# Kernel tuning notes

Hardware: AMD Instinct MI355X
Metric: run time of the kernel (lower is better)

## Reference

```python
import jax, jax.numpy as jnp
import numpy as np

# Mamba2Simple defaults for Mamba2Simple(768, headdim=64)
D_MODEL = 768
D_STATE = 128
D_CONV = 4
EXPAND = 2
HEADDIM = 64
D_INNER = EXPAND * D_MODEL           # 1536
NHEADS = D_INNER // HEADDIM          # 24
CONV_DIM = D_INNER + 2 * D_STATE     # 1792 (x, B, C share the depthwise conv)
D_IN_PROJ = 2 * D_INNER + 2 * D_STATE + NHEADS  # 3352 (z, xBC, dt)
N_LAYERS = 4
IM8 = 64      # 8x8 image tokens
IM64 = 4096   # 64x64 image tokens
L = 1 + IM8 + IM64  # 4161 = s0 + im8 + zoom(im8)
B = 4
EPS = 1e-5


def setup_inputs() -> dict:
    key = jax.random.key(0)
    ks = iter(jax.random.split(key, 40))
    nrm = lambda shape, s=0.02: jax.random.normal(next(ks), shape, jnp.float32) * s
    inp = {
        'im8': jax.random.normal(next(ks), (B, IM8, 3), jnp.float32),
        'im64': jax.random.normal(next(ks), (B, IM64, 3), jnp.float32),
        # RGBToModel / ModelToRGB linear projections
        'from_rgb_w': nrm((3, D_MODEL)),
        'from_rgb_b': jnp.zeros((D_MODEL,), jnp.float32),
        'to_rgb_w': nrm((D_MODEL, 3)),
        'to_rgb_b': jnp.zeros((3,), jnp.float32),
        # learned prefix token and zoom positional suffix
        's0': nrm((1, 1, D_MODEL), 1.0),
        'suffix': nrm((IM64, D_MODEL), 1.0),
        'norm0_w': jnp.ones((D_MODEL,), jnp.float32),
        'norm0_b': jnp.zeros((D_MODEL,), jnp.float32),
        # per-layer (stacked over N_LAYERS) Mamba2 params
        'ln_w': jnp.ones((N_LAYERS, D_MODEL), jnp.float32),
        'ln_b': jnp.zeros((N_LAYERS, D_MODEL), jnp.float32),
        'in_proj_w': nrm((N_LAYERS, D_MODEL, D_IN_PROJ)),
        'conv_w': nrm((N_LAYERS, CONV_DIM, D_CONV), 0.1),
        'conv_b': jnp.zeros((N_LAYERS, CONV_DIM), jnp.float32),
        'dt_bias': nrm((N_LAYERS, NHEADS), 0.1),
        'A_log': jnp.log(jax.random.uniform(next(ks), (N_LAYERS, NHEADS), jnp.float32, 1.0, 16.0)),
        'D': nrm((N_LAYERS, NHEADS), 1.0),
        'gn_w': jnp.ones((N_LAYERS, D_INNER), jnp.float32),
        'out_proj_w': nrm((N_LAYERS, D_INNER, D_MODEL)),
    }
    return inp


def _layernorm(x, w, b):
    mu = jnp.mean(x, axis=-1, keepdims=True)
    var = jnp.mean((x - mu) ** 2, axis=-1, keepdims=True)
    return (x - mu) * jax.lax.rsqrt(var + EPS) * w + b


def _rmsnorm(x, w):
    return x * jax.lax.rsqrt(jnp.mean(x * x, axis=-1, keepdims=True) + EPS) * w


def _causal_conv1d(x, w, b):
    # x: (B, L, C) depthwise causal conv, kernel (C, K)
    xt = x.transpose(0, 2, 1)  # (B, C, L)
    y = jax.lax.conv_general_dilated(
        xt, w[:, None, :], window_strides=(1,), padding=[(D_CONV - 1, 0)],
        dimension_numbers=('NCH', 'OIH', 'NCH'), feature_group_count=w.shape[0])
    return y.transpose(0, 2, 1) + b


def _mamba2(u, Wi, cw, cb, dtb, Alog, Dh, gw, Wo):
    # u: (B, L, d_model)
    Bsz, Ln, _ = u.shape
    zxbcdt = u @ Wi  # (B, L, D_IN_PROJ)
    z = zxbcdt[..., :D_INNER]
    xBC = zxbcdt[..., D_INNER:D_INNER + CONV_DIM]
    dt = jax.nn.softplus(zxbcdt[..., D_INNER + CONV_DIM:] + dtb)  # (B, L, H)
    xBC = jax.nn.silu(_causal_conv1d(xBC, cw, cb))
    x = xBC[..., :D_INNER].reshape(Bsz, Ln, NHEADS, HEADDIM)  # (B,L,H,P)
    Bm = xBC[..., D_INNER:D_INNER + D_STATE]                  # (B,L,N)
    Cm = xBC[..., D_INNER + D_STATE:]                         # (B,L,N)
    A = -jnp.exp(Alog)            # (H,)
    dA = jnp.exp(dt * A)          # (B,L,H) decay factors

    def step(state, inputs):
        # state: (B,H,P,N)
        xt, dtt, dAt, Bt, Ct = inputs
        state = state * dAt[:, :, None, None] + jnp.einsum('bh,bhp,bn->bhpn', dtt, xt, Bt)
        y = jnp.einsum('bhpn,bn->bhp', state, Ct)
        return state, y

    st0 = jnp.zeros((Bsz, NHEADS, HEADDIM, D_STATE), u.dtype)
    xs = (x.transpose(1, 0, 2, 3), dt.transpose(1, 0, 2), dA.transpose(1, 0, 2),
          Bm.transpose(1, 0, 2), Cm.transpose(1, 0, 2))
    _, ys = jax.lax.scan(step, st0, xs)  # ys: (L,B,H,P)
    y = ys.transpose(1, 0, 2, 3) + Dh[None, None, :, None] * x  # D skip per head
    y = y.reshape(Bsz, Ln, D_INNER)
    y = _rmsnorm(y * jax.nn.silu(z), gw)  # RMSNormGated (norm_before_gate=False)
    return y @ Wo


def reference(im8, im64, from_rgb_w, from_rgb_b, to_rgb_w, to_rgb_b, s0, suffix,
              norm0_w, norm0_b, ln_w, ln_b, in_proj_w, conv_w, conv_b,
              dt_bias, A_log, D, gn_w, out_proj_w):
    Bsz = im8.shape[0]
    h8 = im8 @ from_rgb_w + from_rgb_b  # (B,64,d)
    # zoom: each 8x8 pixel repeated into an 8x8 block -> 64x64, plus suffix
    v = h8.reshape(Bsz, 8, 8, D_MODEL)
    zm = jnp.repeat(jnp.repeat(v, 8, axis=1), 8, axis=2).reshape(Bsz, IM64, D_MODEL) + suffix
    x = jnp.concatenate([jnp.broadcast_to(s0, (Bsz, 1, D_MODEL)), h8, zm], axis=1)  # (B,4161,d)
    x = _layernorm(x, norm0_w, norm0_b)
    for i in range(N_LAYERS):
        x = x + _mamba2(_layernorm(x, ln_w[i], ln_b[i]), in_proj_w[i], conv_w[i],
                        conv_b[i], dt_bias[i], A_log[i], D[i], gn_w[i], out_proj_w[i])
    x = x[:, -IM64:]
    y_hat = x @ to_rgb_w + to_rgb_b  # (B,4096,3)
    loss = jnp.mean((y_hat - im64) ** 2)
    return y_hat, loss
```

## Files before the change

### kernel.cpp

```cpp
#include <hip/hip_runtime.h>
#include <hip/hip_bf16.h>
#include <math.h>

#define LTOT 4161
#define BATCH 4
#define NROWS (BATCH*LTOT)
#define NPAD1 3456
#define DM 768
#define DI 1536
#define DIP 3352
#define ZLD 3328
#define NH 24
#define HD 64
#define DS 128
#define EPSF 1e-5f
#define CHK 128
#define NCH 33
#define NBLK (BATCH*NCH*NH)
#define LDF 136
#define XLD 72
#define RLD 264

typedef __attribute__((ext_vector_type(8))) __bf16 bf16x8;
typedef __attribute__((ext_vector_type(4))) float f32x4;
typedef __attribute__((ext_vector_type(8))) short short8;
typedef __attribute__((ext_vector_type(4))) unsigned int u32x4;
typedef unsigned short u16;
typedef unsigned int u32;

static __device__ __forceinline__ u16 f2bf(float f){
  unsigned u = __builtin_bit_cast(unsigned, f);
  u += 0x7FFFu + ((u >> 16) & 1u);
  return (u16)(u >> 16);
}
static __device__ __forceinline__ float bf2f(u16 v){
  return __builtin_bit_cast(float, ((unsigned)v) << 16);
}
static __device__ __forceinline__ float siluf(float v){ return v / (1.f + __expf(-v)); }

static __device__ __forceinline__ int xcd_swz(int orig, int nwg){
  int xcd = orig & 7;
  int idx = orig >> 3;
  int q = nwg >> 3, r = nwg & 7;
  int base = (xcd < r) ? xcd*(q + 1) : r*(q + 1) + (xcd - r)*q;
  return base + idx;
}

__device__ __forceinline__ float blockSum256(float v, float* sh){
  #pragma unroll
  for (int o = 32; o > 0; o >>= 1) v += __shfl_down(v, o);
  int w = threadIdx.x >> 6;
  if ((threadIdx.x & 63) == 0) sh[w] = v;
  __syncthreads();
  v = sh[0] + sh[1] + sh[2] + sh[3];
  __syncthreads();
  return v;
}

__global__ __launch_bounds__(256)
void build_x_kernel(const float* __restrict__ im8, const float* __restrict__ frw,
                    const float* __restrict__ frb, const float* __restrict__ s0,
                    const float* __restrict__ suffix, const float* __restrict__ w,
                    const float* __restrict__ bb, float* __restrict__ x)
{
  int row = blockIdx.x;
  int b = row / LTOT, l = row % LTOT;
  int t = threadIdx.x;
  __shared__ float sh[4];
  float v[3];
  if (l == 0) {
    #pragma unroll
    for (int i = 0; i < 3; i++) v[i] = s0[t + i*256];
  } else if (l <= 64) {
    int p = l - 1;
    float r0 = im8[(b*64 + p)*3 + 0], r1 = im8[(b*64 + p)*3 + 1], r2 = im8[(b*64 + p)*3 + 2];
    #pragma unroll
    for (int i = 0; i < 3; i++) {
      int d = t + i*256;
      v[i] = r0*frw[d] + r1*frw[768 + d] + r2*frw[1536 + d] + frb[d];
    }
  } else {
    int j = l - 65;
    int p = ((j >> 9) << 3) | ((j & 63) >> 3);
    float r0 = im8[(b*64 + p)*3 + 0], r1 = im8[(b*64 + p)*3 + 1], r2 = im8[(b*64 + p)*3 + 2];
    #pragma unroll
    for (int i = 0; i < 3; i++) {
      int d = t + i*256;
      v[i] = r0*frw[d] + r1*frw[768 + d] + r2*frw[1536 + d] + frb[d] + suffix[(size_t)j*768 + d];
    }
  }
  float s = v[0] + v[1] + v[2];
  s = blockSum256(s, sh);
  float mu = s * (1.f/768.f);
  float q = 0;
  #pragma unroll
  for (int i = 0; i < 3; i++) { float d = v[i] - mu; q += d*d; }
  q = blockSum256(q, sh);
  float rs = rsqrtf(q * (1.f/768.f) + EPSF);
  float* xr = x + (size_t)row*DM;
  #pragma unroll
  for (int i = 0; i < 3; i++) {
    int d = t + i*256;
    xr[d] = (v[i] - mu)*rs*w[d] + bb[d];
  }
}

__global__ __launch_bounds__(256)
void ln_bf16_kernel(const float* __restrict__ x, const float* __restrict__ w,
                    const float* __restrict__ bb, u16* __restrict__ out,
                    float* __restrict__ ssq)
{
  int row = blockIdx.x;
  int t = threadIdx.x;
  __shared__ float sh[4];
  const float* xr = x + (size_t)row*DM;
  float v[3];
  #pragma unroll
  for (int i = 0; i < 3; i++) v[i] = xr[t + i*256];
  if (t == 0) ssq[row] = 0.f;
  float s = v[0] + v[1] + v[2];
  s = blockSum256(s, sh);
  float mu = s * (1.f/768.f);
  float q = 0;
  #pragma unroll
  for (int i = 0; i < 3; i++) { float d = v[i] - mu; q += d*d; }
  q = blockSum256(q, sh);
  float rs = rsqrtf(q * (1.f/768.f) + EPSF);
  u16* orow = out + (size_t)row*DM;
  #pragma unroll
  for (int i = 0; i < 3; i++) {
    int d = t + i*256;
    orow[d] = f2bf((v[i] - mu)*rs*w[d] + bb[d]);
  }
}

__global__ __launch_bounds__(256)
void transp_bf16(const float* __restrict__ in, u16* __restrict__ out, int K, int N)
{
  __shared__ float tl[32][33];
  int tx = threadIdx.x & 31, ty = threadIdx.x >> 5;
  int n0 = blockIdx.x * 32, k0 = blockIdx.y * 32;
  #pragma unroll
  for (int r = 0; r < 4; r++) {
    int k = k0 + ty + r*8, n = n0 + tx;
    tl[ty + r*8][tx] = (n < N) ? in[(size_t)k*N + n] : 0.f;
  }
  __syncthreads();
  #pragma unroll
  for (int r = 0; r < 4; r++) {
    int n = n0 + ty + r*8, k = k0 + tx;
    out[(size_t)n*K + k] = f2bf(tl[tx][ty + r*8]);
  }
}

#define LD8(p) (*(const short8*)(p))

__global__ __launch_bounds__(256)
void gemm0(const u16* __restrict__ A, const u16* __restrict__ BT,
           u16* __restrict__ zxO, const float* __restrict__ dtbias,
           float* __restrict__ dtO)
{
  __shared__ __align__(16) u16 As[2][128*40];
  __shared__ __align__(16) u16 Bs[2][128*40];
  const int t = threadIdx.x;
  const int nid = xcd_swz(blockIdx.y*27 + blockIdx.x, 27*131);
  const int bm = nid / 27, bn = nid % 27;
  const int lane = t & 63, wave = t >> 6;
  const int wr = wave >> 1, wc = wave & 1;
  const int r16 = lane & 15, kb = lane >> 4;

  const int m = t >> 1, half = t & 1;
  const int grow = bm*128 + m;
  const bool valid = grow < NROWS;
  const u16* gA = A + (size_t)(valid ? grow : 0)*DM + half*16;
  const u16* gB = BT + (size_t)(bn*128 + m)*DM + half*16;
  const int wofs = m*40 + half*16;

  short8 a0 = {}, a1 = {}, b0, b1;
  b0 = LD8(gB); b1 = LD8(gB + 8);
  if (valid) { a0 = LD8(gA); a1 = LD8(gA + 8); }
  *(short8*)&As[0][wofs] = a0; *(short8*)&As[0][wofs + 8] = a1;
  *(short8*)&Bs[0][wofs] = b0; *(short8*)&Bs[0][wofs + 8] = b1;
  __syncthreads();

  f32x4 acc[4][4] = {};
  int p = 0;
  for (int kt = 0; kt < DM; kt += 32) {
    const bool more = (kt + 32 < DM);
    if (more) {
      b0 = LD8(gB + kt + 32); b1 = LD8(gB + kt + 40);
      if (valid) { a0 = LD8(gA + kt + 32); a1 = LD8(gA + kt + 40); }
    }
    bf16x8 af[4], bfr[4];
    #pragma unroll
    for (int i = 0; i < 4; i++) af[i]  = *(const bf16x8*)&As[p][(wr*64 + i*16 + r16)*40 + kb*8];
    #pragma unroll
    for (int i = 0; i < 4; i++) bfr[i] = *(const bf16x8*)&Bs[p][(wc*64 + i*16 + r16)*40 + kb*8];
    #pragma unroll
    for (int i = 0; i < 4; i++)
      #pragma unroll
      for (int j = 0; j < 4; j++)
        acc[i][j] = __builtin_amdgcn_mfma_f32_16x16x32_bf16(af[i], bfr[j], acc[i][j], 0, 0, 0);
    if (more) {
      *(short8*)&As[p^1][wofs] = a0; *(short8*)&As[p^1][wofs + 8] = a1;
      *(short8*)&Bs[p^1][wofs] = b0; *(short8*)&Bs[p^1][wofs + 8] = b1;
    }
    __syncthreads();
    p ^= 1;
  }
  const int rbase = bm*128 + wr*64, cbase = bn*128 + wc*64;
  #pragma unroll
  for (int i = 0; i < 4; i++) {
    #pragma unroll
    for (int j = 0; j < 4; j++) {
      int col = cbase + j*16 + r16;
      #pragma unroll
      for (int e = 0; e < 4; e++) {
        int row = rbase + i*16 + kb*4 + e;
        if (row < NROWS) {
          float v = acc[i][j][e];
          if (col < ZLD) {
            zxO[(size_t)row*ZLD + col] = f2bf(v);
          } else if (col < DIP) {
            int hh = col - ZLD;
            float d = v + dtbias[hh];
            d = (d > 20.f) ? d : log1pf(expf(d));
            dtO[(size_t)row*NH + hh] = d;
          }
        }
      }
    }
  }
}

__global__ __launch_bounds__(256)
void gemm_out(const u16* __restrict__ A, const float* __restrict__ ssq,
              const float* __restrict__ gw, const u16* __restrict__ BT,
              float* __restrict__ X)
{
  __shared__ __align__(16) u16 As[2][128*40];
  __shared__ __align__(16) u16 Bs[2][128*40];
  __shared__ float gwl[DI];
  const int t = threadIdx.x;
  const int nid = xcd_swz(blockIdx.y*6 + blockIdx.x, 6*131);
  const int bm = nid / 6, bn = nid % 6;
  const int lane = t & 63, wave = t >> 6;
  const int wr = wave >> 1, wc = wave & 1;
  const int r16 = lane & 15, kb = lane >> 4;

  for (int i = t; i < DI; i += 256) gwl[i] = gw[i];

  const int m = t >> 1, half = t & 1;
  const int grow = bm*128 + m;
  const bool valid = grow < NROWS;
  const float rs = valid ? rsqrtf(ssq[grow] * (1.f/1536.f) + EPSF) : 0.f;
  const u16* gA = A + (size_t)(valid ? grow : 0)*ZLD + half*16;
  const u16* gB = BT + (size_t)(bn*128 + m)*DI + half*16;
  const int wofs = m*40 + half*16;

  short8 ra0 = {}, ra1 = {}, b0, b1;
  b0 = LD8(gB); b1 = LD8(gB + 8);
  if (valid) { ra0 = LD8(gA); ra1 = LD8(gA + 8); }
  __syncthreads();
  {
    const int c0 = half*16;
    short8 ta0, ta1;
    #pragma unroll
    for (int j = 0; j < 8; j++) ta0[j] = (short)f2bf(bf2f((u16)ra0[j]) * rs * gwl[c0 + j]);
    #pragma unroll
    for (int j = 0; j < 8; j++) ta1[j] = (short)f2bf(bf2f((u16)ra1[j]) * rs * gwl[c0 + 8 + j]);
    *(short8*)&As[0][wofs] = ta0; *(short8*)&As[0][wofs + 8] = ta1;
    *(short8*)&Bs[0][wofs] = b0;  *(short8*)&Bs[0][wofs + 8] = b1;
  }
  __syncthreads();

  f32x4 acc[4][4] = {};
  int p = 0;
  for (int kt = 0; kt < DI; kt += 32) {
    const bool more = (kt + 32 < DI);
    if (more) {
      b0 = LD8(gB + kt + 32); b1 = LD8(gB + kt + 40);
      if (valid) { ra0 = LD8(gA + kt + 32); ra1 = LD8(gA + kt + 40); }
    }
    bf16x8 af[4], bfr[4];
    #pragma unroll
    for (int i = 0; i < 4; i++) af[i]  = *(const bf16x8*)&As[p][(wr*64 + i*16 + r16)*40 + kb*8];
    #pragma unroll
    for (int i = 0; i < 4; i++) bfr[i] = *(const bf16x8*)&Bs[p][(wc*64 + i*16 + r16)*40 + kb*8];
    #pragma unroll
    for (int i = 0; i < 4; i++)
      #pragma unroll
      for (int j = 0; j < 4; j++)
        acc[i][j] = __builtin_amdgcn_mfma_f32_16x16x32_bf16(af[i], bfr[j], acc[i][j], 0, 0, 0);
    if (more) {
      const int c0 = kt + 32 + half*16;
      short8 ta0, ta1;
      #pragma unroll
      for (int j = 0; j < 8; j++) ta0[j] = (short)f2bf(bf2f((u16)ra0[j]) * rs * gwl[c0 + j]);
      #pragma unroll
      for (int j = 0; j < 8; j++) ta1[j] = (short)f2bf(bf2f((u16)ra1[j]) * rs * gwl[c0 + 8 + j]);
      *(short8*)&As[p^1][wofs] = ta0; *(short8*)&As[p^1][wofs + 8] = ta1;
      *(short8*)&Bs[p^1][wofs] = b0;  *(short8*)&Bs[p^1][wofs + 8] = b1;
    }
    __syncthreads();
    p ^= 1;
  }
  const int rbase = bm*128 + wr*64, cbase = bn*128 + wc*64;
  #pragma unroll
  for (int i = 0; i < 4; i++) {
    #pragma unroll
    for (int j = 0; j < 4; j++) {
      int col = cbase + j*16 + r16;
      #pragma unroll
      for (int e = 0; e < 4; e++) {
        int row = rbase + i*16 + kb*4 + e;
        if (row < NROWS) X[(size_t)row*DM + col] += acc[i][j][e];
      }
    }
  }
}


__global__ __launch_bounds__(128)
void dtcs_kernel(const float* __restrict__ dt, const float* __restrict__ alog,
                 float* __restrict__ csb, float* __restrict__ dtvb,
                 float* __restrict__ wjsb, float* __restrict__ dtot)
{
  const int id = blockIdx.x;
  const int h = id % NH; const int c = (id / NH) % NCH; const int b = id / (NH*NCH);
  const int t = threadIdx.x;
  const int base = c*CHK;
  int rows = LTOT - base; if (rows > CHK) rows = CHK;
  __shared__ float cs[128];
  float dv = 0.f;
  if (t < rows) dv = dt[(size_t)(b*LTOT + base + t)*NH + h];
  const float aexp = __expf(alog[h]);
  cs[t] = -dv * aexp;
  __syncthreads();
  for (int off = 1; off < 128; off <<= 1) {
    float add = (t >= off) ? cs[t - off] : 0.f;
    __syncthreads();
    cs[t] += add;
    __syncthreads();
  }
  float csl = cs[127];
  size_t o = (size_t)id*128 + t;
  csb[o] = cs[t];
  dtvb[o] = dv;
  wjsb[o] = __expf(csl - cs[t]) * dv;
  if (t == 0) dtot[id] = __expf(csl);
}

__global__ __launch_bounds__(512)
void convBC_kernel(const u16* __restrict__ zx, const float* __restrict__ cw,
                   const float* __restrict__ cb, u16* __restrict__ Ccv,
                   u16* __restrict__ BcvT, u16* __restrict__ Sraw)
{
  const int bc = xcd_swz(blockIdx.x, BATCH*NCH);
  const int b = bc / NCH, c = bc % NCH;
  const int t = threadIdx.x;
  const int base = c*CHK;
  __shared__ __align__(16) u16 raw[131*RLD + 8];
  __shared__ __align__(16) u16 Bt[128*LDF];
  __shared__ __align__(16) u16 Ct[128*LDF];
  const u16* zb = zx + (size_t)(b*LTOT)*ZLD;

  #pragma unroll
  for (int rg = 0; rg < 9; rg++) {
    int idx = rg*512 + t;
    int r = idx >> 5, seg = idx & 31;
    if (r < 131) {
      int g = base - 3 + r;
      short8 v = {};
      if (g >= 0 && g < LTOT) v = LD8(zb + (size_t)g*ZLD + 3072 + seg*8);
      *(short8*)&raw[r*RLD + seg*8] = v;
    }
  }
  __syncthreads();
  {
    const int cht = t & 255, halfj = t >> 8;
    const int isC = cht >> 7, n = cht & 127;
    const int ch = 1536 + cht;
    float w0 = cw[ch*4+0], w1 = cw[ch*4+1], w2 = cw[ch*4+2], w3 = cw[ch*4+3];
    float bias = cb[ch];
    const int rb = halfj*64;
    float r0 = bf2f(raw[(rb+0)*RLD + cht]);
    float r1 = bf2f(raw[(rb+1)*RLD + cht]);
    float r2 = bf2f(raw[(rb+2)*RLD + cht]);
    u16* dstT = isC ? Ct : Bt;
    #pragma unroll 4
    for (int j = 0; j < 64; j++) {
      float r3 = bf2f(raw[(rb + j + 3)*RLD + cht]);
      float o = bias + w0*r0 + w1*r1 + w2*r2 + w3*r3;
      dstT[(rb + j)*LDF + n] = f2bf(siluf(o));
      r0 = r1; r1 = r2; r2 = r3;
    }
  }
  __syncthreads();
  #pragma unroll
  for (int rg = 0; rg < 4; rg++) {
    int idx = rg*512 + t;
    int r = idx >> 4, seg = idx & 15;
    int g = base + r;
    if (g < LTOT)
      *(short8*)(Ccv + (size_t)(b*LTOT + g)*128 + seg*8) = *(const short8*)&Ct[r*LDF + seg*8];
  }
  u16* bT = BcvT + (size_t)bc*16384;
  #pragma unroll
  for (int rg = 0; rg < 4; rg++) {
    int idx = rg*512 + t;
    int n = idx >> 4, js = (idx & 15)*8;
    short8 v;
    #pragma unroll
    for (int k = 0; k < 8; k++) v[k] = (short)Bt[(js + k)*LDF + n];
    *(short8*)(bT + n*128 + js) = v;
  }
  {
    const int lane = t & 63, wave = t >> 6;
    const int r16 = lane & 15, kb = lane >> 4;
    f32x4 acc[8] = {};
    #pragma unroll
    for (int kt = 0; kt < 4; kt++) {
      bf16x8 af = *(const bf16x8*)&Ct[(wave*16 + r16)*LDF + kt*32 + kb*8];
      #pragma unroll
      for (int nj = 0; nj < 8; nj++) {
        bf16x8 bfr = *(const bf16x8*)&Bt[(nj*16 + r16)*LDF + kt*32 + kb*8];
        acc[nj] = __builtin_amdgcn_mfma_f32_16x16x32_bf16(af, bfr, acc[nj], 0, 0, 0);
      }
    }
    u16* sdst = Sraw + (size_t)bc*16384;
    #pragma unroll
    for (int nj = 0; nj < 8; nj++)
      #pragma unroll
      for (int e = 0; e < 4; e++) {
        int i = wave*16 + kb*4 + e;
        int j = nj*16 + r16;
        sdst[i*128 + j] = f2bf(acc[nj][e]);
      }
  }
}

__global__ __launch_bounds__(256)
void chunk_state_kernel(const u16* __restrict__ zx, const float* __restrict__ wjsb,
                        const float* __restrict__ cw, const float* __restrict__ cb,
                        const u16* __restrict__ BcvT, u16* __restrict__ cstat)
{
  const int id = xcd_swz(blockIdx.x, NBLK);
  const int h = id % NH; const int c = (id / NH) % NCH; const int b = id / (NH*NCH);
  const int t = threadIdx.x;
  const int base = c*CHK;

  __shared__ __align__(16) u16 Bbuf[128*LDF];
  __shared__ __align__(16) u16 xbuf[131*XLD + 8];
  __shared__ float wjs[128];

  const u16* zb = zx + (size_t)(b*LTOT)*ZLD;
  if (t < 128) wjs[t] = wjsb[(size_t)id*128 + t];
  {
    const u16* bT = BcvT + (size_t)(b*NCH + c)*16384;
    #pragma unroll
    for (int rg = 0; rg < 8; rg++) {
      int idx = rg*256 + t;
      int n = idx >> 4, js = (idx & 15)*8;
      *(short8*)&Bbuf[n*LDF + js] = LD8(bT + n*128 + js);
    }
  }
  #pragma unroll
  for (int rg = 0; rg < 5; rg++) {
    int r = rg*32 + (t >> 3);
    int seg = t & 7;
    if (r < 131) {
      int g = base - 3 + r;
      short8 v = {};
      if (g >= 0 && g < LTOT) v = LD8(zb + (size_t)g*ZLD + 1536 + h*HD + seg*8);
      *(short8*)&xbuf[r*XLD + seg*8] = v;
    }
  }
  __syncthreads();

  const int p_ = t & 63, jq = t >> 6;
  u32 pkx[16];
  {
    const int ch = h*HD + p_;
    float w0 = cw[ch*4+0], w1 = cw[ch*4+1], w2 = cw[ch*4+2], w3 = cw[ch*4+3];
    float bias = cb[ch];
    const int rb = jq*32;
    float r0 = bf2f(xbuf[(rb+0)*XLD + p_]);
    float r1 = bf2f(xbuf[(rb+1)*XLD + p_]);
    float r2 = bf2f(xbuf[(rb+2)*XLD + p_]);
    #pragma unroll
    for (int k2 = 0; k2 < 16; k2++) {
      float r3 = bf2f(xbuf[(rb + 2*k2 + 3)*XLD + p_]);
      float o0 = bias + w0*r0 + w1*r1 + w2*r2 + w3*r3;
      float r4 = bf2f(xbuf[(rb + 2*k2 + 4)*XLD + p_]);
      float o1 = bias + w0*r1 + w1*r2 + w2*r3 + w3*r4;
      float s0 = siluf(o0) * wjs[rb + 2*k2];
      float s1 = siluf(o1) * wjs[rb + 2*k2 + 1];
      pkx[k2] = (u32)f2bf(s0) | ((u32)f2bf(s1) << 16);
      r0 = r2; r1 = r3; r2 = r4;
    }
  }
  __syncthreads();
  #pragma unroll
  for (int q = 0; q < 4; q++) {
    u32x4 v; v[0] = pkx[q*4]; v[1] = pkx[q*4+1]; v[2] = pkx[q*4+2]; v[3] = pkx[q*4+3];
    *(u32x4*)&xbuf[p_*LDF + jq*32 + q*8] = v;
  }
  __syncthreads();

  const int lane = t & 63, wave = t >> 6;
  const int r16 = lane & 15, kb = lane >> 4;
  const int n0 = wave*32;
  f32x4 acc[4][2] = {};
  #pragma unroll
  for (int kt = 0; kt < 4; kt++) {
    bf16x8 af[4], bfr[2];
    #pragma unroll
    for (int m = 0; m < 4; m++) af[m] = *(const bf16x8*)&xbuf[(m*16 + r16)*LDF + kt*32 + kb*8];
    #pragma unroll
    for (int nn = 0; nn < 2; nn++) bfr[nn] = *(const bf16x8*)&Bbuf[(n0 + nn*16 + r16)*LDF + kt*32 + kb*8];
    #pragma unroll
    for (int m = 0; m < 4; m++)
      #pragma unroll
      for (int nn = 0; nn < 2; nn++)
        acc[m][nn] = __builtin_amdgcn_mfma_f32_16x16x32_bf16(af[m], bfr[nn], acc[m][nn], 0, 0, 0);
  }
  u16* dst = cstat + (size_t)id*64*128;
  #pragma unroll
  for (int m = 0; m < 4; m++)
    #pragma unroll
    for (int nn = 0; nn < 2; nn++)
      #pragma unroll
      for (int e = 0; e < 4; e++) {
        int p = m*16 + kb*4 + e;
        int n = n0 + nn*16 + r16;
        dst[p*128 + n] = f2bf(acc[m][nn][e]);
      }
}

__global__ __launch_bounds__(256)
void state_scan_kernel(u16* __restrict__ cstat, const float* __restrict__ dtot)
{
  const int blk = blockIdx.x;
  const int b = blk / (NH*4);
  const int rest = blk % (NH*4);
  const int h = rest >> 2, sec = rest & 3;
  const int t = threadIdx.x;
  const int eofs = sec*2048 + t*8;
  float run[8];
  #pragma unroll
  for (int k = 0; k < 8; k++) run[k] = 0.f;
  size_t id0 = (size_t)(b*NCH)*NH + h;
  short8 cur = LD8(cstat + id0*8192 + eofs);
  float d = dtot[id0];
  for (int c = 0; c < NCH; ++c) {
    size_t id = (size_t)(b*NCH + c)*NH + h;
    u16* slab = cstat + id*8192 + eofs;
    short8 nxt = {}; float nd = 0.f;
    if (c + 1 < NCH) {
      nxt = LD8(slab + (size_t)NH*8192);
      nd = dtot[id + NH];
    }
    short8 out;
    #pragma unroll
    for (int k = 0; k < 8; k++) {
      float csv = bf2f((u16)cur[k]);
      out[k] = (short)f2bf(run[k]);
      run[k] = run[k]*d + csv;
    }
    *(short8*)slab = out;
    cur = nxt;
    d = nd;
  }
}

__global__ __launch_bounds__(512, 4)
void chunk_output_kernel(u16* __restrict__ zx, const float* __restrict__ csb,
                         const float* __restrict__ dtvb, const float* __restrict__ cw,
                         const float* __restrict__ cb, const float* __restrict__ Dvec,
                         const u16* __restrict__ Sraw, const u16* __restrict__ Ccv,
                         const u16* __restrict__ cstat, float* __restrict__ ssq)
{
  const int id = xcd_swz(blockIdx.x, NBLK);
  const int h = id % NH; const int c = (id / NH) % NCH; const int b = id / (NH*NCH);
  const int t = threadIdx.x;
  const int base = c*CHK;
  int rows = LTOT - base; if (rows > CHK) rows = CHK;

  __shared__ __align__(16) u16 Bc[128*LDF];
  __shared__ __align__(16) u16 stT[64*LDF];
  __shared__ __align__(16) u16 xbuf[131*XLD + 8];
  __shared__ float dtv[128];
  __shared__ float cs[128];

  const u16* zb = zx + (size_t)(b*LTOT)*ZLD;
  const size_t crow0 = (size_t)(b*LTOT)*128;
  if (t < 128) {
    cs[t]  = csb[(size_t)id*128 + t];
    dtv[t] = dtvb[(size_t)id*128 + t];
  }
  {
    const u16* slab = cstat + (size_t)id*8192;
    int p = t >> 3, nb = (t & 7)*16;
    *(short8*)&stT[p*LDF + nb]     = LD8(slab + p*128 + nb);
    *(short8*)&stT[p*LDF + nb + 8] = LD8(slab + p*128 + nb + 8);
  }
  #pragma unroll
  for (int rg = 0; rg < 3; rg++) {
    int r = rg*64 + (t >> 3);
    int seg = t & 7;
    if (r < 131) {
      int g = base - 3 + r;
      short8 v = {};
      if (g >= 0 && g < LTOT) v = LD8(zb + (size_t)g*ZLD + 1536 + h*HD + seg*8);
      *(short8*)&xbuf[r*XLD + seg*8] = v;
    }
  }
  __syncthreads();

  const int p_ = t & 63, jq = t >> 6;
  u32 pkx[8];
  {
    const int ch = h*HD + p_;
    float w0 = cw[ch*4+0], w1 = cw[ch*4+1], w2 = cw[ch*4+2], w3 = cw[ch*4+3];
    float bias = cb[ch];
    const int rb = jq*16;
    float r0 = bf2f(xbuf[(rb+0)*XLD + p_]);
    float r1 = bf2f(xbuf[(rb+1)*XLD + p_]);
    float r2 = bf2f(xbuf[(rb+2)*XLD + p_]);
    #pragma unroll
    for (int k2 = 0; k2 < 8; k2++) {
      float r3 = bf2f(xbuf[(rb + 2*k2 + 3)*XLD + p_]);
      float o0 = bias + w0*r0 + w1*r1 + w2*r2 + w3*r3;
      float r4 = bf2f(xbuf[(rb + 2*k2 + 4)*XLD + p_]);
      float o1 = bias + w0*r1 + w1*r2 + w2*r3 + w3*r4;
      int j0 = rb + 2*k2;
      u32 lo = (j0     < rows) ? (u32)f2bf(siluf(o0)) : 0u;
      u32 hi = (j0 + 1 < rows) ? (u32)f2bf(siluf(o1)) : 0u;
      pkx[k2] = lo | (hi << 16);
      r0 = r2; r1 = r3; r2 = r4;
    }
  }
  {
    const u16* sS = Sraw + (size_t)(b*NCH + c)*16384;
    #pragma unroll
    for (int q = 0; q < 4; q++) {
      int idx = q*512 + t;
      int i = idx >> 4, seg = (idx & 15)*8;
      short8 s = LD8(sS + i*128 + seg);
      float csi = cs[i];
      short8 o;
      #pragma unroll
      for (int k = 0; k < 8; k++) {
        int j = seg + k;
        float f = 0.f;
        if (j <= i && i < rows) f = __expf(csi - cs[j]) * dtv[j];
        o[k] = (short)f2bf(bf2f((u16)s[k]) * f);
      }
      *(short8*)&Bc[i*LDF + seg] = o;
    }
  }
  __syncthreads();
  {
    u32x4 v0; v0[0] = pkx[0]; v0[1] = pkx[1]; v0[2] = pkx[2]; v0[3] = pkx[3];
    u32x4 v1; v1[0] = pkx[4]; v1[1] = pkx[5]; v1[2] = pkx[6]; v1[3] = pkx[7];
    *(u32x4*)&xbuf[p_*LDF + jq*16]     = v0;
    *(u32x4*)&xbuf[p_*LDF + jq*16 + 8] = v1;
  }
  __syncthreads();

  const int lane = t & 63, wave = t >> 6;
  const int r16 = lane & 15, kb = lane >> 4;

  {
    const int iq = wave;
    bf16x8 cF[4];
    {
      int i = iq*16 + r16;
      int g = base + i; if (g >= LTOT) g = base;
      #pragma unroll
      for (int kt = 0; kt < 4; kt++)
        cF[kt] = *(const bf16x8*)(Ccv + crow0 + (size_t)g*128 + kt*32 + kb*8);
    }
    f32x4 accY[4] = {};
    #pragma unroll
    for (int kt = 0; kt < 4; kt++) {
      bf16x8 af = *(const bf16x8*)&Bc[(iq*16 + r16)*LDF + kt*32 + kb*8];
      #pragma unroll
      for (int n = 0; n < 4; n++) {
        bf16x8 bfr = *(const bf16x8*)&xbuf[(n*16 + r16)*LDF + kt*32 + kb*8];
        accY[n] = __builtin_amdgcn_mfma_f32_16x16x32_bf16(af, bfr, accY[n], 0, 0, 0);
      }
    }
    f32x4 accS[4] = {};
    #pragma unroll
    for (int kt = 0; kt < 4; kt++) {
      #pragma unroll
      for (int n = 0; n < 4; n++) {
        bf16x8 bfr = *(const bf16x8*)&stT[(n*16 + r16)*LDF + kt*32 + kb*8];
        accS[n] = __builtin_amdgcn_mfma_f32_16x16x32_bf16(cF[kt], bfr, accS[n], 0, 0, 0);
      }
    }
    const float dcoef = Dvec[h];
    #pragma unroll
    for (int e = 0; e < 4; e++) {
      int i = iq*16 + kb*4 + e;
      if (i < rows) {
        float sc = __expf(cs[i]);
        size_t orow = (size_t)(b*LTOT + base + i)*ZLD + h*HD;
        float g2 = 0.f;
        #pragma unroll
        for (int n = 0; n < 4; n++) {
          int p = n*16 + r16;
          float xv = bf2f(xbuf[p*LDF + i]);
          float yv = accY[n][e] + sc*accS[n][e] + dcoef*xv;
          float gv = yv * siluf(bf2f(zx[orow + p]));
          zx[orow + p] = f2bf(gv);
          g2 += gv*gv;
        }
        g2 += __shfl_xor(g2, 1);
        g2 += __shfl_xor(g2, 2);
        g2 += __shfl_xor(g2, 4);
        g2 += __shfl_xor(g2, 8);
        if (r16 == 0) atomicAdd(&ssq[b*LTOT + base + i], g2);
      }
    }
  }
}

__global__ __launch_bounds__(256)
void head_kernel(const float* __restrict__ x, const float* __restrict__ tw,
                 const float* __restrict__ tb, const float* __restrict__ im64,
                 float* __restrict__ out, float* __restrict__ partial)
{
  int bj = blockIdx.x;
  int b = bj >> 12, j = bj & 4095;
  int row = b*LTOT + 65 + j;
  const float* xr = x + (size_t)row*DM;
  int t = threadIdx.x;
  float p0 = 0, p1 = 0, p2 = 0;
  for (int k = t; k < 768; k += 256) {
    float xv = xr[k];
    p0 += xv*tw[k*3 + 0]; p1 += xv*tw[k*3 + 1]; p2 += xv*tw[k*3 + 2];
  }
  __shared__ float sh[4];
  p0 = blockSum256(p0, sh);
  p1 = blockSum256(p1, sh);
  p2 = blockSum256(p2, sh);
  if (t == 0) {
    float y0 = p0 + tb[0], y1 = p1 + tb[1], y2 = p2 + tb[2];
    size_t o = (size_t)bj*3;
    out[o] = y0; out[o + 1] = y1; out[o + 2] = y2;
    float d0 = y0 - im64[o], d1 = y1 - im64[o + 1], d2 = y2 - im64[o + 2];
    partial[bj] = d0*d0 + d1*d1 + d2*d2;
  }
}

__global__ __launch_bounds__(256)
void loss_reduce(const float* __restrict__ partial, float* __restrict__ out)
{
  int t = threadIdx.x;
  float s = 0.f;
  for (int i = t; i < BATCH*4096; i += 256) s += partial[i];
  __shared__ float sh[4];
  s = blockSum256(s, sh);
  if (t == 0) out[49152] = s * (1.f/49152.f);
}

static inline size_t alignup(size_t v){ return (v + 255) & ~(size_t)255; }

extern "C" void kernel_launch(void* const* d_in, const int* in_sizes, int n_in,
                              void* d_out, int out_size, void* d_ws, size_t ws_size,
                              hipStream_t stream)
{
  const float* im8        = (const float*)d_in[0];
  const float* im64       = (const float*)d_in[1];
  const float* from_rgb_w = (const float*)d_in[2];
  const float* from_rgb_b = (const float*)d_in[3];
  const float* to_rgb_w   = (const float*)d_in[4];
  const float* to_rgb_b   = (const float*)d_in[5];
  const float* s0         = (const float*)d_in[6];
  const float* suffix     = (const float*)d_in[7];
  const float* norm0_w    = (const float*)d_in[8];
  const float* norm0_b    = (const float*)d_in[9];
  const float* ln_w       = (const float*)d_in[10];
  const float* ln_b       = (const float*)d_in[11];
  const float* in_proj_w  = (const float*)d_in[12];
  const float* conv_w     = (const float*)d_in[13];
  const float* conv_b     = (const float*)d_in[14];
  const float* dt_bias    = (const float*)d_in[15];
  const float* A_log      = (const float*)d_in[16];
  const float* Dvec       = (const float*)d_in[17];
  const float* gn_w       = (const float*)d_in[18];
  const float* out_proj_w = (const float*)d_in[19];

  char* w = (char*)d_ws;
  size_t off = 0;
  float* x     = (float*)(w + off); off = alignup(off + (size_t)NROWS*DM*4);
  u16*   zx    = (u16*)  (w + off); off = alignup(off + (size_t)NROWS*ZLD*2);
  u16*   scr   = (u16*)  (w + off); off = alignup(off + (size_t)NBLK*64*128*2);
  u16*   Sraw  = (u16*)  (w + off); off = alignup(off + (size_t)BATCH*NCH*16384*2);
  u16*   Ccv   = (u16*)  (w + off); off = alignup(off + (size_t)NROWS*128*2);
  u16*   BcvT  = (u16*)  (w + off); off = alignup(off + (size_t)BATCH*NCH*16384*2);
  float* dt    = (float*)(w + off); off = alignup(off + (size_t)NROWS*NH*4);
  float* csb   = (float*)(w + off); off = alignup(off + (size_t)NBLK*128*4);
  float* dtvb  = (float*)(w + off); off = alignup(off + (size_t)NBLK*128*4);
  float* wjsb  = (float*)(w + off); off = alignup(off + (size_t)NBLK*128*4);
  float* ssq   = (float*)(w + off); off = alignup(off + (size_t)NROWS*4);
  float* dtot  = (float*)(w + off); off = alignup(off + (size_t)NBLK*4);
  float* lpart = (float*)(w + off); off = alignup(off + (size_t)BATCH*4096*4);
  u16* wT    = scr;
  u16* xn    = (u16*)((char*)scr + alignup((size_t)NPAD1*DM*2));
  u16* cstat = scr;

  build_x_kernel<<<NROWS, 256, 0, stream>>>(im8, from_rgb_w, from_rgb_b, s0, suffix,
                                            norm0_w, norm0_b, x);

  for (int i = 0; i < 4; i++) {
    ln_bf16_kernel<<<NROWS, 256, 0, stream>>>(x, ln_w + i*DM, ln_b + i*DM, xn, ssq);
    transp_bf16<<<dim3(NPAD1/32, DM/32), 256, 0, stream>>>(in_proj_w + (size_t)i*DM*DIP, wT, DM, DIP);
    gemm0<<<dim3(27, 131), 256, 0, stream>>>(xn, wT, zx, dt_bias + i*NH, dt);
    dtcs_kernel<<<NBLK, 128, 0, stream>>>(dt, A_log + i*NH, csb, dtvb, wjsb, dtot);
    convBC_kernel<<<BATCH*NCH, 512, 0, stream>>>(zx, conv_w + (size_t)i*(DI+2*DS)*4,
        conv_b + i*(DI+2*DS), Ccv, BcvT, Sraw);
    chunk_state_kernel<<<NBLK, 256, 0, stream>>>(zx, wjsb,
        conv_w + (size_t)i*(DI+2*DS)*4, conv_b + i*(DI+2*DS), BcvT, cstat);
    state_scan_kernel<<<BATCH*NH*4, 256, 0, stream>>>(cstat, dtot);
    chunk_output_kernel<<<NBLK, 512, 0, stream>>>(zx, csb, dtvb,
        conv_w + (size_t)i*(DI+2*DS)*4, conv_b + i*(DI+2*DS), Dvec + i*NH, Sraw, Ccv, cstat, ssq);
    transp_bf16<<<dim3(DM/32, DI/32), 256, 0, stream>>>(out_proj_w + (size_t)i*DI*DM, wT, DI, DM);
    gemm_out<<<dim3(6, 131), 256, 0, stream>>>(zx, ssq, gn_w + i*DI, wT, x);
  }

  head_kernel<<<BATCH*4096, 256, 0, stream>>>(x, to_rgb_w, to_rgb_b, im64, (float*)d_out, lpart);
  loss_reduce<<<1, 256, 0, stream>>>(lpart, (float*)d_out);
}
```

Measured before the change: 1.986 ms.

## Load MFMA operands directly from global, drop LDS staging, regroup gemm0 tiles

```diff
diff --git a/kernel.cpp b/kernel.cpp
--- a/kernel.cpp
+++ b/kernel.cpp
@@ -164,7 +164,9 @@
   __shared__ __align__(16) u16 Bs[2][128*40];
   const int t = threadIdx.x;
   const int nid = xcd_swz(blockIdx.y*27 + blockIdx.x, 27*131);
-  const int bm = nid / 27, bn = nid % 27;
+  const int sc = nid / (131*9);
+  const int rr = nid % (131*9);
+  const int bm = rr / 9, bn = sc*9 + rr % 9;
   const int lane = t & 63, wave = t >> 6;
   const int wr = wave >> 1, wc = wave & 1;
   const int r16 = lane & 15, kb = lane >> 4;
@@ -450,21 +452,11 @@
   const int t = threadIdx.x;
   const int base = c*CHK;
 
-  __shared__ __align__(16) u16 Bbuf[128*LDF];
   __shared__ __align__(16) u16 xbuf[131*XLD + 8];
   __shared__ float wjs[128];
 
   const u16* zb = zx + (size_t)(b*LTOT)*ZLD;
   if (t < 128) wjs[t] = wjsb[(size_t)id*128 + t];
-  {
-    const u16* bT = BcvT + (size_t)(b*NCH + c)*16384;
-    #pragma unroll
-    for (int rg = 0; rg < 8; rg++) {
-      int idx = rg*256 + t;
-      int n = idx >> 4, js = (idx & 15)*8;
-      *(short8*)&Bbuf[n*LDF + js] = LD8(bT + n*128 + js);
-    }
-  }
   #pragma unroll
   for (int rg = 0; rg < 5; rg++) {
     int r = rg*32 + (t >> 3);
@@ -511,6 +503,7 @@
   const int lane = t & 63, wave = t >> 6;
   const int r16 = lane & 15, kb = lane >> 4;
   const int n0 = wave*32;
+  const u16* bT = BcvT + (size_t)(b*NCH + c)*16384;
   f32x4 acc[4][2] = {};
   #pragma unroll
   for (int kt = 0; kt < 4; kt++) {
@@ -518,7 +511,8 @@
     #pragma unroll
     for (int m = 0; m < 4; m++) af[m] = *(const bf16x8*)&xbuf[(m*16 + r16)*LDF + kt*32 + kb*8];
     #pragma unroll
-    for (int nn = 0; nn < 2; nn++) bfr[nn] = *(const bf16x8*)&Bbuf[(n0 + nn*16 + r16)*LDF + kt*32 + kb*8];
+    for (int nn = 0; nn < 2; nn++)
+      bfr[nn] = *(const bf16x8*)(bT + (n0 + nn*16 + r16)*128 + kt*32 + kb*8);
     #pragma unroll
     for (int m = 0; m < 4; m++)
       #pragma unroll
@@ -587,7 +581,6 @@
   const int base = c*CHK;
   int rows = LTOT - base; if (rows > CHK) rows = CHK;
 
-  __shared__ __align__(16) u16 Bc[128*LDF];
   __shared__ __align__(16) u16 stT[64*LDF];
   __shared__ __align__(16) u16 xbuf[131*XLD + 8];
   __shared__ float dtv[128];
@@ -641,25 +634,6 @@
       r0 = r2; r1 = r3; r2 = r4;
     }
   }
-  {
-    const u16* sS = Sraw + (size_t)(b*NCH + c)*16384;
-    #pragma unroll
-    for (int q = 0; q < 4; q++) {
-      int idx = q*512 + t;
-      int i = idx >> 4, seg = (idx & 15)*8;
-      short8 s = LD8(sS + i*128 + seg);
-      float csi = cs[i];
-      short8 o;
-      #pragma unroll
-      for (int k = 0; k < 8; k++) {
-        int j = seg + k;
-        float f = 0.f;
-        if (j <= i && i < rows) f = __expf(csi - cs[j]) * dtv[j];
-        o[k] = (short)f2bf(bf2f((u16)s[k]) * f);
-      }
-      *(short8*)&Bc[i*LDF + seg] = o;
-    }
-  }
   __syncthreads();
   {
     u32x4 v0; v0[0] = pkx[0]; v0[1] = pkx[1]; v0[2] = pkx[2]; v0[3] = pkx[3];
@@ -674,10 +648,13 @@
 
   {
     const int iq = wave;
+    const int i_ = iq*16 + r16;
+    const float csi = cs[i_];
+    const bool irow = (i_ < rows);
+    const u16* sSrow = Sraw + (size_t)(b*NCH + c)*16384 + i_*128;
     bf16x8 cF[4];
     {
-      int i = iq*16 + r16;
-      int g = base + i; if (g >= LTOT) g = base;
+      int g = base + i_; if (g >= LTOT) g = base;
       #pragma unroll
       for (int kt = 0; kt < 4; kt++)
         cF[kt] = *(const bf16x8*)(Ccv + crow0 + (size_t)g*128 + kt*32 + kb*8);
@@ -685,7 +662,18 @@
     f32x4 accY[4] = {};
     #pragma unroll
     for (int kt = 0; kt < 4; kt++) {
-      bf16x8 af = *(const bf16x8*)&Bc[(iq*16 + r16)*LDF + kt*32 + kb*8];
+      const int cbase0 = kt*32 + kb*8;
+      short8 pa = {};
+      if (irow && cbase0 <= i_) {
+        short8 s = LD8(sSrow + cbase0);
+        #pragma unroll
+        for (int k = 0; k < 8; k++) {
+          int jj = cbase0 + k;
+          float f = (jj <= i_) ? __expf(csi - cs[jj]) * dtv[jj] : 0.f;
+          pa[k] = (short)f2bf(bf2f((u16)s[k]) * f);
+        }
+      }
+      bf16x8 af = __builtin_bit_cast(bf16x8, pa);
       #pragma unroll
       for (int n = 0; n < 4; n++) {
         bf16x8 bfr = *(const bf16x8*)&xbuf[(n*16 + r16)*LDF + kt*32 + kb*8];
```

New measurement: 1.809 ms, median of 2. 8.9% less time.
